# Kernel optimization log

Measured on AMD Instinct MI355X. Metric: run time of the kernel, lower is better.

The kernel has to match this reference:

```python
import jax, jax.numpy as jnp
import numpy as np

N, E, F, DH, R = 50000, 800000, 128, 128, 6  # nodes, edges, in-feat, hidden, relations (heads=1)
EPS = 1e-5
NEG_SLOPE = 0.01


def setup_inputs() -> dict:
    key = jax.random.key(0)
    ks = jax.random.split(key, 20)
    sF = 1.0 / np.sqrt(F)
    sD = 1.0 / np.sqrt(DH)
    return {
        "x": jax.random.normal(ks[0], (N, F), dtype=jnp.float32),
        "edge_index": jax.random.randint(ks[1], (2, E), 0, N, dtype=jnp.int64),
        "edge_type": jax.random.randint(ks[2], (E,), 0, R, dtype=jnp.int64),
        # RGCNConv params
        "rgcn_w": jax.random.normal(ks[3], (R, F, DH), dtype=jnp.float32) * sF,
        "rgcn_root": jax.random.normal(ks[4], (F, DH), dtype=jnp.float32) * sF,
        "rgcn_bias": jnp.zeros((DH,), dtype=jnp.float32),
        # TransformerConv params (heads=1, concat=True)
        "wq": jax.random.normal(ks[5], (DH, DH), dtype=jnp.float32) * sD,
        "bq": jnp.zeros((DH,), dtype=jnp.float32),
        "wk": jax.random.normal(ks[6], (DH, DH), dtype=jnp.float32) * sD,
        "bk": jnp.zeros((DH,), dtype=jnp.float32),
        "wv": jax.random.normal(ks[7], (DH, DH), dtype=jnp.float32) * sD,
        "bv": jnp.zeros((DH,), dtype=jnp.float32),
        "wskip": jax.random.normal(ks[8], (DH, DH), dtype=jnp.float32) * sD,
        "bskip": jnp.zeros((DH,), dtype=jnp.float32),
        # BatchNorm1d params (training-mode batch stats)
        "bn_gamma": jnp.ones((DH,), dtype=jnp.float32),
        "bn_beta": jnp.zeros((DH,), dtype=jnp.float32),
    }


def _rgcn(x, src, dst, edge_type, w, root, bias):
    # PyG RGCNConv: per-relation mean aggregation of x_j @ W_r over incoming edges, + root + bias
    out = x @ root + bias  # [N, DH]
    for r in range(R):
        m = (edge_type == r)
        xw = x @ w[r]  # [N, DH]
        msg = jnp.where(m[:, None], xw[src], 0.0)  # [E, DH]
        s = jax.ops.segment_sum(msg, dst, num_segments=N)
        cnt = jax.ops.segment_sum(m.astype(x.dtype), dst, num_segments=N)
        out = out + s / jnp.maximum(cnt, 1.0)[:, None]
    return out


def _transformer_conv(x, src, dst, wq, bq, wk, bk, wv, bv, wskip, bskip):
    # PyG TransformerConv, heads=1: edge-softmax attention over incoming edges + skip projection
    q = x @ wq + bq  # [N, DH]
    k = x @ wk + bk
    v = x @ wv + bv
    score = jnp.sum(q[dst] * k[src], axis=-1) / jnp.sqrt(jnp.asarray(DH, x.dtype))  # [E]
    smax = jax.ops.segment_max(score, dst, num_segments=N)  # -inf for empty segments (unused)
    a = jnp.exp(score - smax[dst])
    denom = jax.ops.segment_sum(a, dst, num_segments=N)
    alpha = a / denom[dst]  # every edge's dst has >=1 edge, denom > 0
    agg = jax.ops.segment_sum(alpha[:, None] * v[src], dst, num_segments=N)  # [N, DH]
    return agg + (x @ wskip + bskip)


def reference(x, edge_index, edge_type, rgcn_w, rgcn_root, rgcn_bias,
              wq, bq, wk, bk, wv, bv, wskip, bskip, bn_gamma, bn_beta):
    src, dst = edge_index[0], edge_index[1]
    h = _rgcn(x, src, dst, edge_type, rgcn_w, rgcn_root, rgcn_bias)
    h = _transformer_conv(h, src, dst, wq, bq, wk, bk, wv, bv, wskip, bskip)
    # BatchNorm1d (training: batch statistics, biased variance)
    mu = jnp.mean(h, axis=0)
    var = jnp.mean(jnp.square(h - mu), axis=0)
    h = bn_gamma * (h - mu) * jax.lax.rsqrt(var + EPS) + bn_beta
    return jnp.where(h > 0, h, NEG_SLOPE * h)
```

## Files before the change

### kernel.cpp

```cpp
#include <hip/hip_runtime.h>
#include <hip/hip_bf16.h>
#include <math.h>

#define FDIM 128
#define NREL 6

typedef _Float16 half8 __attribute__((ext_vector_type(8)));
typedef _Float16 h16x2 __attribute__((ext_vector_type(2)));
typedef float f32x4 __attribute__((ext_vector_type(4)));

#if __has_builtin(__builtin_amdgcn_fdot2)
#define FDOT2(A, B, C) __builtin_amdgcn_fdot2((A), (B), (C), false)
#else
#define FDOT2(A, B, C) ((float)(A)[0] * (float)(B)[0] + ((float)(A)[1] * (float)(B)[1] + (C)))
#endif

static __device__ __forceinline__ unsigned short f2h(float f) {
  union { _Float16 h; unsigned short u; } p; p.h = (_Float16)f; return p.u;
}

__global__ void cvt_x_kernel(const float* __restrict__ x, unsigned short* __restrict__ xh,
                             int n4) {
  int i = blockIdx.x * 256 + threadIdx.x;
  if (i < n4) {
    float4 v = ((const float4*)x)[i];
    union { _Float16 h[4]; uint2 u; } p;
    p.h[0] = (_Float16)v.x; p.h[1] = (_Float16)v.y;
    p.h[2] = (_Float16)v.z; p.h[3] = (_Float16)v.w;
    ((uint2*)xh)[i] = p.u;
  }
}

__global__ void cvt_wr_kernel(const float* __restrict__ root, const float* __restrict__ w,
                              unsigned short* __restrict__ bt) {
  int i = blockIdx.x * 256 + threadIdx.x;
  if (i < 896 * 128) {
    int n = i / 896, kk = i - n * 896;
    float v = (kk < 128) ? root[kk * 128 + n] : w[(long long)(kk - 128) * 128 + n];
    bt[i] = f2h(v);
  }
}

struct WPtrs { const float* W[4]; };
__global__ void cvt_wq_kernel(WPtrs wp, unsigned short* __restrict__ bt) {
  int i = blockIdx.x * 256 + threadIdx.x;
  if (i < 4 * 128 * 128) {
    int z = i >> 14;
    int r = i & 16383;
    int n = r >> 7, kk = r & 127;
    bt[i] = f2h(wp.W[z][kk * 128 + n]);
  }
}

struct GArgs {
  const unsigned short* Ax;
  const unsigned short* Aagg;
  const unsigned short* Bt;
  const float* bias[4];
  unsigned short* qh; unsigned short* kh; unsigned short* vh; float* sk;
  unsigned short* h;
  int M, K;
};

template <int MODE>
__launch_bounds__(256)
__global__ void gemm_mfma(GArgs g) {
  __shared__ unsigned short Ah[64 * 64];
  __shared__ unsigned short Bh[128 * 64];
  const int tid = threadIdx.x;
  const int lane = tid & 63;
  const int wid = tid >> 6;
  const int wm = wid >> 1, wn = wid & 1;
  const int lr = lane & 15, lk = lane >> 4;
  const int m0 = blockIdx.x * 64;
  const int z = (MODE == 1) ? blockIdx.z : 0;
  const unsigned short* Bt = g.Bt + (long long)z * 128 * g.K;
  const int K = g.K;
  const int M = g.M;

  f32x4 acc[2][4];
#pragma unroll
  for (int a = 0; a < 2; ++a)
#pragma unroll
    for (int b = 0; b < 4; ++b) { acc[a][b][0] = 0.f; acc[a][b][1] = 0.f; acc[a][b][2] = 0.f; acc[a][b][3] = 0.f; }

  for (int k0 = 0; k0 < K; k0 += 64) {
    __syncthreads();
#pragma unroll
    for (int p = 0; p < 2; ++p) {
      int idx = tid + 256 * p;
      int r = idx >> 3, c = idx & 7;
      int row = m0 + r; if (row > M - 1) row = M - 1;
      const unsigned short* srcp;
      if (MODE == 0)
        srcp = (k0 < 128) ? (g.Ax + (long long)row * 128 + k0 + c * 8)
                          : (g.Aagg + (long long)row * 768 + (k0 - 128) + c * 8);
      else
        srcp = g.Ax + (long long)row * 128 + k0 + c * 8;
      uint4 u = *(const uint4*)srcp;
      ((uint4*)Ah)[r * 8 + (c ^ (r & 7))] = u;
    }
#pragma unroll
    for (int p = 0; p < 4; ++p) {
      int idx = tid + 256 * p;
      int rn = idx >> 3, c = idx & 7;
      uint4 u = *(const uint4*)(Bt + (long long)rn * K + k0 + c * 8);
      ((uint4*)Bh)[rn * 8 + (c ^ (rn & 7))] = u;
    }
    __syncthreads();
#pragma unroll
    for (int ks = 0; ks < 2; ++ks) {
      half8 a[2], b[4];
#pragma unroll
      for (int fm = 0; fm < 2; ++fm) {
        int row = wm * 32 + fm * 16 + lr;
        a[fm] = *(const half8*)&((uint4*)Ah)[row * 8 + ((ks * 4 + lk) ^ (row & 7))];
      }
#pragma unroll
      for (int fn = 0; fn < 4; ++fn) {
        int col = wn * 64 + fn * 16 + lr;
        b[fn] = *(const half8*)&((uint4*)Bh)[col * 8 + ((ks * 4 + lk) ^ (col & 7))];
      }
#pragma unroll
      for (int fm = 0; fm < 2; ++fm)
#pragma unroll
        for (int fn = 0; fn < 4; ++fn)
          acc[fm][fn] = __builtin_amdgcn_mfma_f32_16x16x32_f16(a[fm], b[fn], acc[fm][fn], 0, 0, 0);
    }
  }

  const float CF = 0.08838834764831845f * 1.4426950408889634f;
  const float* bias = (MODE == 0) ? g.bias[0] : g.bias[z];
#pragma unroll
  for (int fm = 0; fm < 2; ++fm) {
#pragma unroll
    for (int fn = 0; fn < 4; ++fn) {
      int col = wn * 64 + fn * 16 + lr;
      float bv = bias[col];
#pragma unroll
      for (int j = 0; j < 4; ++j) {
        int row = m0 + wm * 32 + fm * 16 + lk * 4 + j;
        if (row < M) {
          float vv = acc[fm][fn][j] + bv;
          long long off = (long long)row * 128 + col;
          if (MODE == 0) {
            g.h[off] = f2h(vv);
          } else {
            if (z == 0) g.qh[off] = f2h(vv * CF);
            else if (z == 1) g.kh[off] = f2h(vv);
            else if (z == 2) g.vh[off] = f2h(vv);
            else g.sk[off] = vv;
          }
        }
      }
    }
  }
}

__global__ void hist_kernel(const int* __restrict__ dst, int* __restrict__ deg, int E) {
  int e = blockIdx.x * blockDim.x + threadIdx.x;
  if (e < E) atomicAdd(&deg[dst[e]], 1);
}

__launch_bounds__(1024)
__global__ void scan1(const int* __restrict__ deg, int* __restrict__ incl,
                      int* __restrict__ part, int n) {
  __shared__ int sh[1024];
  int tid = threadIdx.x;
  int i = blockIdx.x * 1024 + tid;
  sh[tid] = (i < n) ? deg[i] : 0;
  __syncthreads();
  for (int o = 1; o < 1024; o <<= 1) {
    int t = (tid >= o) ? sh[tid - o] : 0;
    __syncthreads();
    sh[tid] += t;
    __syncthreads();
  }
  if (i < n) incl[i] = sh[tid];
  if (tid == 1023) part[blockIdx.x] = sh[1023];
}

__global__ void scan2(int* part, int nb) {
  int lane = threadIdx.x;
  int run = 0;
  for (int b0 = 0; b0 < nb; b0 += 64) {
    int i = b0 + lane;
    int orig = (i < nb) ? part[i] : 0;
    int v = orig;
#pragma unroll
    for (int o = 1; o < 64; o <<= 1) {
      int t = __shfl_up(v, o);
      if (lane >= o) v += t;
    }
    if (i < nb) part[i] = run + v - orig;
    run += __shfl(v, 63);
  }
}

__global__ void scan3(const int* __restrict__ incl, const int* __restrict__ part,
                      int* __restrict__ offs, int n) {
  int i = blockIdx.x * blockDim.x + threadIdx.x;
  if (i < n) {
    offs[i + 1] = incl[i] + part[i >> 10];
    if (i == 0) offs[0] = 0;
  }
}

__global__ void scatter_kernel(const int* __restrict__ src, const int* __restrict__ dst,
                               const int* __restrict__ etype, const int* __restrict__ offs,
                               int* __restrict__ cur, int* __restrict__ csrc,
                               int* __restrict__ ctyp, int E) {
  int e = blockIdx.x * blockDim.x + threadIdx.x;
  if (e < E) {
    int d = dst[e];
    int p = offs[d] + atomicAdd(&cur[d], 1);
    csrc[p] = src[e];
    ctyp[p] = etype[e];
  }
}

__launch_bounds__(256)
__global__ void rgcn_agg(const unsigned short* __restrict__ xh, const int* __restrict__ offs,
                         const int* __restrict__ csrc, const int* __restrict__ ctyp,
                         unsigned short* __restrict__ aggh, int N) {
  int node = blockIdx.x * 4 + (threadIdx.x >> 6);
  if (node >= N) return;
  int lane = threadIdx.x & 63;
  int start = offs[node], end = offs[node + 1];

  float a0x = 0.f, a0y = 0.f, a1x = 0.f, a1y = 0.f, a2x = 0.f, a2y = 0.f;
  float a3x = 0.f, a3y = 0.f, a4x = 0.f, a4y = 0.f, a5x = 0.f, a5y = 0.f;
  int c0 = 0, c1 = 0, c2 = 0, c3 = 0, c4 = 0, c5 = 0;

#define ACC(T, XU)                                                         \
  {                                                                        \
    union { unsigned u; _Float16 h[2]; } cc; cc.u = (XU);                  \
    float fx = (float)cc.h[0], fy = (float)cc.h[1];                        \
    switch (T) {                                                           \
      case 0: a0x += fx; a0y += fy; ++c0; break;                           \
      case 1: a1x += fx; a1y += fy; ++c1; break;                           \
      case 2: a2x += fx; a2y += fy; ++c2; break;                           \
      case 3: a3x += fx; a3y += fy; ++c3; break;                           \
      case 4: a4x += fx; a4y += fy; ++c4; break;                           \
      default: a5x += fx; a5y += fy; ++c5; break;                          \
    }                                                                      \
  }

  int e = start;
  for (; e + 4 <= end; e += 4) {
    int s0 = csrc[e], s1 = csrc[e + 1], s2 = csrc[e + 2], s3 = csrc[e + 3];
    int t0 = __builtin_amdgcn_readfirstlane(ctyp[e]);
    int t1 = __builtin_amdgcn_readfirstlane(ctyp[e + 1]);
    int t2 = __builtin_amdgcn_readfirstlane(ctyp[e + 2]);
    int t3 = __builtin_amdgcn_readfirstlane(ctyp[e + 3]);
    unsigned x0 = ((const unsigned*)(xh + (long long)s0 * FDIM))[lane];
    unsigned x1 = ((const unsigned*)(xh + (long long)s1 * FDIM))[lane];
    unsigned x2 = ((const unsigned*)(xh + (long long)s2 * FDIM))[lane];
    unsigned x3 = ((const unsigned*)(xh + (long long)s3 * FDIM))[lane];
    ACC(t0, x0) ACC(t1, x1) ACC(t2, x2) ACC(t3, x3)
  }
  for (; e < end; ++e) {
    int s0 = csrc[e];
    int t0 = __builtin_amdgcn_readfirstlane(ctyp[e]);
    unsigned x0 = ((const unsigned*)(xh + (long long)s0 * FDIM))[lane];
    ACC(t0, x0)
  }
#undef ACC

  float i0 = c0 ? 1.f / (float)c0 : 0.f;
  float i1 = c1 ? 1.f / (float)c1 : 0.f;
  float i2 = c2 ? 1.f / (float)c2 : 0.f;
  float i3 = c3 ? 1.f / (float)c3 : 0.f;
  float i4 = c4 ? 1.f / (float)c4 : 0.f;
  float i5 = c5 ? 1.f / (float)c5 : 0.f;
  unsigned* ap = (unsigned*)(aggh + (long long)node * (NREL * FDIM));
  union { _Float16 h[2]; unsigned u; } p;
#define WR(ri, AX, AY, IV) { p.h[0] = (_Float16)((AX) * (IV)); p.h[1] = (_Float16)((AY) * (IV)); ap[(ri) * 64 + lane] = p.u; }
  WR(0, a0x, a0y, i0) WR(1, a1x, a1y, i1) WR(2, a2x, a2y, i2)
  WR(3, a3x, a3y, i3) WR(4, a4x, a4y, i4) WR(5, a5x, a5y, i5)
#undef WR
}

__launch_bounds__(256)
__global__ void attn_kernel(const unsigned short* __restrict__ qh,
                            const unsigned short* __restrict__ kh,
                            const unsigned short* __restrict__ vh,
                            const int* __restrict__ offs, const int* __restrict__ csrc,
                            float* __restrict__ out, int N) {
  int node = blockIdx.x * 4 + (threadIdx.x >> 6);
  if (node >= N) return;
  int lane = threadIdx.x & 63;
  int start = offs[node], end = offs[node + 1];
  int deg = end - start;
  if (deg <= 0) return;

  const int g16 = lane >> 4;
  const int f = lane & 15;

  union U4 { uint4 u; h16x2 h[4]; };
  U4 qf; qf.u = *(const uint4*)(qh + (long long)node * FDIM + f * 8);

  float m = -INFINITY, den = 0.f, acc0 = 0.f, acc1 = 0.f;

#define LOADQ(E0, S0, S1, S2, S3, KU, V0, V1, V2, V3)                        \
  {                                                                          \
    S0 = csrc[(E0) + (g16 ^ 0)];                                             \
    S1 = csrc[(E0) + (g16 ^ 1)];                                             \
    S2 = csrc[(E0) + (g16 ^ 2)];                                             \
    S3 = csrc[(E0) + (g16 ^ 3)];                                             \
    KU = *(const uint4*)(kh + (long long)S0 * FDIM + f * 8);                 \
    V0 = ((const unsigned*)(vh + (long long)S0 * FDIM))[lane];               \
    V1 = ((const unsigned*)(vh + (long long)S1 * FDIM))[lane];               \
    V2 = ((const unsigned*)(vh + (long long)S2 * FDIM))[lane];               \
    V3 = ((const unsigned*)(vh + (long long)S3 * FDIM))[lane];               \
  }

#define PROCESS(KU, V0, V1, V2, V3, MASKED, M0, M1, M2, M3)                  \
  {                                                                          \
    U4 kf; kf.u = KU;                                                        \
    float pd = FDOT2(qf.h[0], kf.h[0], 0.f);                                 \
    pd = FDOT2(qf.h[1], kf.h[1], pd);                                        \
    pd = FDOT2(qf.h[2], kf.h[2], pd);                                        \
    pd = FDOT2(qf.h[3], kf.h[3], pd);                                        \
    pd += __shfl_xor(pd, 1);  pd += __shfl_xor(pd, 2);                       \
    pd += __shfl_xor(pd, 4);  pd += __shfl_xor(pd, 8);                       \
    float sc0 = pd;                                        \
    float sc1 = __shfl_xor(pd, 16);                        \
    float sc2 = __shfl_xor(pd, 32);                        \
    float sc3 = __shfl_xor(pd, 48);                        \
    if (MASKED) {                                                            \
      if (!(M0)) sc0 = -INFINITY;                                            \
      if (!(M1)) sc1 = -INFINITY;                                            \
      if (!(M2)) sc2 = -INFINITY;                                            \
      if (!(M3)) sc3 = -INFINITY;                                            \
    }                                                                        \
    float mx = fmaxf(fmaxf(sc0, sc1), fmaxf(sc2, sc3));                      \
    float mn = fmaxf(m, mx);                                                 \
    float scl = exp2f(m - mn);                                               \
    float a0 = exp2f(sc0 - mn), a1 = exp2f(sc1 - mn);                        \
    float a2 = exp2f(sc2 - mn), a3 = exp2f(sc3 - mn);                        \
    den = den * scl + ((a0 + a1) + (a2 + a3));                               \
    union { unsigned u; _Float16 h[2]; } w0, w1, w2, w3;                     \
    w0.u = V0; w1.u = V1; w2.u = V2; w3.u = V3;                              \
    acc0 = acc0 * scl + a0 * (float)w0.h[0] + a1 * (float)w1.h[0]            \
                      + a2 * (float)w2.h[0] + a3 * (float)w3.h[0];           \
    acc1 = acc1 * scl + a0 * (float)w0.h[1] + a1 * (float)w1.h[1]            \
                      + a2 * (float)w2.h[1] + a3 * (float)w3.h[1];           \
    m = mn;                                                                  \
  }

  int nfull4 = deg & ~3;
  int e = start;
  if (nfull4 > 0) {
    int sA0, sA1, sA2, sA3; uint4 kA; unsigned vA0, vA1, vA2, vA3;
    LOADQ(e, sA0, sA1, sA2, sA3, kA, vA0, vA1, vA2, vA3)
    for (; e < start + nfull4; e += 4) {
      int sB0, sB1, sB2, sB3; uint4 kB; unsigned vB0, vB1, vB2, vB3;
      bool more = (e + 4 < start + nfull4);
      if (more) LOADQ(e + 4, sB0, sB1, sB2, sB3, kB, vB0, vB1, vB2, vB3)
      PROCESS(kA, vA0, vA1, vA2, vA3, false, 1, 1, 1, 1)
      if (more) { kA = kB; vA0 = vB0; vA1 = vB1; vA2 = vB2; vA3 = vB3; }
    }
  }
  int rem = deg & 3;
  if (rem) {
    int e0 = start + nfull4;
    int j0 = g16 ^ 0, j1 = g16 ^ 1, j2 = g16 ^ 2, j3 = g16 ^ 3;
    int sT0 = csrc[e0 + (j0 < rem ? j0 : 0)];
    int sT1 = csrc[e0 + (j1 < rem ? j1 : 0)];
    int sT2 = csrc[e0 + (j2 < rem ? j2 : 0)];
    int sT3 = csrc[e0 + (j3 < rem ? j3 : 0)];
    uint4 kT = *(const uint4*)(kh + (long long)sT0 * FDIM + f * 8);
    unsigned vT0 = ((const unsigned*)(vh + (long long)sT0 * FDIM))[lane];
    unsigned vT1 = ((const unsigned*)(vh + (long long)sT1 * FDIM))[lane];
    unsigned vT2 = ((const unsigned*)(vh + (long long)sT2 * FDIM))[lane];
    unsigned vT3 = ((const unsigned*)(vh + (long long)sT3 * FDIM))[lane];
    PROCESS(kT, vT0, vT1, vT2, vT3, true, j0 < rem, j1 < rem, j2 < rem, j3 < rem)
  }
#undef LOADQ
#undef PROCESS

  float inv = 1.f / den;
  float2* op = (float2*)(out + (long long)node * FDIM);
  float2 o = op[lane];
  o.x += acc0 * inv;
  o.y += acc1 * inv;
  op[lane] = o;
}

__launch_bounds__(128)
__global__ void bn_stats(const float* __restrict__ x, float* __restrict__ gsum,
                         float* __restrict__ gsq, int N) {
  int d = threadIdx.x;
  float s = 0.f, qq = 0.f;
  for (int r = blockIdx.x; r < N; r += gridDim.x) {
    float vv = x[(long long)r * FDIM + d];
    s += vv;
    qq += vv * vv;
  }
  atomicAdd(&gsum[d], s);
  atomicAdd(&gsq[d], qq);
}

__global__ void bn_final(const float* __restrict__ gsum, const float* __restrict__ gsq,
                         const float* __restrict__ gamma, const float* __restrict__ beta,
                         float* __restrict__ ss, int N) {
  int d = threadIdx.x;
  if (d < FDIM) {
    float mean = gsum[d] / (float)N;
    float var = gsq[d] / (float)N - mean * mean;
    var = fmaxf(var, 0.f);
    float sc = gamma[d] * rsqrtf(var + 1e-5f);
    ss[d] = sc;
    ss[FDIM + d] = beta[d] - mean * sc;
  }
}

__global__ void bn_apply(float* __restrict__ x, const float* __restrict__ ss, long long total4) {
  long long i = (long long)blockIdx.x * blockDim.x + threadIdx.x;
  if (i < total4) {
    int d0 = (int)((i * 4) & (FDIM - 1));
    float4 vv = ((const float4*)x)[i];
    float y0 = ss[d0 + 0] * vv.x + ss[FDIM + d0 + 0];
    float y1 = ss[d0 + 1] * vv.y + ss[FDIM + d0 + 1];
    float y2 = ss[d0 + 2] * vv.z + ss[FDIM + d0 + 2];
    float y3 = ss[d0 + 3] * vv.w + ss[FDIM + d0 + 3];
    vv.x = (y0 > 0.f) ? y0 : 0.01f * y0;
    vv.y = (y1 > 0.f) ? y1 : 0.01f * y1;
    vv.z = (y2 > 0.f) ? y2 : 0.01f * y2;
    vv.w = (y3 > 0.f) ? y3 : 0.01f * y3;
    ((float4*)x)[i] = vv;
  }
}

extern "C" void kernel_launch(void* const* d_in, const int* in_sizes, int n_in,
                              void* d_out, int out_size, void* d_ws, size_t ws_size,
                              hipStream_t stream) {
  const float* x         = (const float*)d_in[0];
  const int*   ei        = (const int*)d_in[1];
  const int*   etype     = (const int*)d_in[2];
  const float* rgcn_w    = (const float*)d_in[3];
  const float* rgcn_root = (const float*)d_in[4];
  const float* rgcn_bias = (const float*)d_in[5];
  const float* wq = (const float*)d_in[6];  const float* bq = (const float*)d_in[7];
  const float* wk = (const float*)d_in[8];  const float* bk = (const float*)d_in[9];
  const float* wv = (const float*)d_in[10]; const float* bv = (const float*)d_in[11];
  const float* wsk = (const float*)d_in[12]; const float* bsk = (const float*)d_in[13];
  const float* gamma = (const float*)d_in[14]; const float* beta = (const float*)d_in[15];

  const int N = in_sizes[0] / FDIM;
  const int E = in_sizes[1] / 2;
  const int* src = ei;
  const int* dst = ei + E;

  char* base = (char*)d_ws;
  size_t off = 0;
  auto alloc = [&](size_t bytes) -> char* {
    char* p = base + off;
    off += (bytes + 255) & ~(size_t)255;
    return p;
  };
  unsigned short* aggh = (unsigned short*)alloc((size_t)N * (NREL * FDIM) * 2);
  unsigned short* qbuf = aggh;
  unsigned short* kbuf = aggh + (size_t)N * FDIM;
  unsigned short* vbuf = aggh + 2 * (size_t)N * FDIM;
  unsigned short* xh   = (unsigned short*)alloc((size_t)N * FDIM * 2);
  unsigned short* hh   = (unsigned short*)alloc((size_t)N * FDIM * 2);
  unsigned short* btR  = (unsigned short*)alloc((size_t)896 * 128 * 2);
  unsigned short* btQ  = (unsigned short*)alloc((size_t)4 * 128 * 128 * 2);
  int* deg  = (int*)alloc((size_t)2 * N * 4);
  int* cur  = deg + N;
  int* offs = (int*)alloc((size_t)(N + 1) * 4);
  int* incl = (int*)alloc((size_t)N * 4);
  int* part = (int*)alloc((size_t)64 * 4);
  int* csrc = (int*)alloc((size_t)E * 4);
  int* ctyp = (int*)alloc((size_t)E * 4);
  float* gsum = (float*)alloc((size_t)(128 + 128 + 256) * 4);
  float* gsq  = gsum + FDIM;
  float* ss   = gsum + 2 * FDIM;

  float* out = (float*)d_out;

  hipMemsetAsync(deg, 0, (size_t)2 * N * sizeof(int), stream);
  hipMemsetAsync(gsum, 0, (size_t)2 * FDIM * sizeof(float), stream);

  int n4 = N * FDIM / 4;
  cvt_x_kernel<<<(n4 + 255) / 256, 256, 0, stream>>>(x, xh, n4);
  cvt_wr_kernel<<<(896 * 128 + 255) / 256, 256, 0, stream>>>(rgcn_root, rgcn_w, btR);
  WPtrs wp; wp.W[0] = wq; wp.W[1] = wk; wp.W[2] = wv; wp.W[3] = wsk;
  cvt_wq_kernel<<<(4 * 128 * 128 + 255) / 256, 256, 0, stream>>>(wp, btQ);

  hist_kernel<<<(E + 255) / 256, 256, 0, stream>>>(dst, deg, E);
  int nb = (N + 1023) / 1024;
  scan1<<<nb, 1024, 0, stream>>>(deg, incl, part, N);
  scan2<<<1, 64, 0, stream>>>(part, nb);
  scan3<<<(N + 255) / 256, 256, 0, stream>>>(incl, part, offs, N);
  scatter_kernel<<<(E + 255) / 256, 256, 0, stream>>>(src, dst, etype, offs, cur, csrc, ctyp, E);

  const int nodeBlocks = (N + 3) / 4;
  const int gemmBlocks = (N + 63) / 64;

  rgcn_agg<<<nodeBlocks, 256, 0, stream>>>(xh, offs, csrc, ctyp, aggh, N);

  GArgs g0 = {};
  g0.Ax = xh; g0.Aagg = aggh; g0.Bt = btR;
  g0.bias[0] = rgcn_bias;
  g0.h = hh; g0.M = N; g0.K = 896;
  gemm_mfma<0><<<dim3(gemmBlocks, 1, 1), 256, 0, stream>>>(g0);

  GArgs g1 = {};
  g1.Ax = hh; g1.Bt = btQ;
  g1.bias[0] = bq; g1.bias[1] = bk; g1.bias[2] = bv; g1.bias[3] = bsk;
  g1.qh = qbuf; g1.kh = kbuf; g1.vh = vbuf; g1.sk = out;
  g1.M = N; g1.K = 128;
  gemm_mfma<1><<<dim3(gemmBlocks, 1, 4), 256, 0, stream>>>(g1);

  attn_kernel<<<nodeBlocks, 256, 0, stream>>>(qbuf, kbuf, vbuf, offs, csrc, out, N);

  bn_stats<<<512, 128, 0, stream>>>(out, gsum, gsq, N);
  bn_final<<<1, 128, 0, stream>>>(gsum, gsq, gamma, beta, ss, N);
  long long total4 = (long long)N * FDIM / 4;
  bn_apply<<<(int)((total4 + 255) / 256), 256, 0, stream>>>(out, ss, total4);
}
```

Measured before the change: 356.4 us.

## Sort CSR by (dst, relation) and aggregate per-relation segments without type array

The edge CSR is now keyed by destination node times relation, so the histogram, scan and scatter run over N*6 buckets and the per-edge type array is dropped. The RGCN aggregation walks each relation's contiguous segment with a two-deep software prefetch of gathered rows. This removes the per-edge type load and the switch over six accumulator pairs. In exchange the count and scan arrays grow sixfold, the scan grows to about 300 blocks, and scan2 must handle up to 512 partials with a single 64-thread block.

After: 374.3 us. 5.0% more time.

```diff
diff --git a/kernel.cpp b/kernel.cpp
--- a/kernel.cpp
+++ b/kernel.cpp
@@ -157,9 +157,10 @@
   }
 }
 
-__global__ void hist_kernel(const int* __restrict__ dst, int* __restrict__ deg, int E) {
+__global__ void hist_kernel(const int* __restrict__ dst, const int* __restrict__ etype,
+                            int* __restrict__ cnt, int E) {
   int e = blockIdx.x * blockDim.x + threadIdx.x;
-  if (e < E) atomicAdd(&deg[dst[e]], 1);
+  if (e < E) atomicAdd(&cnt[dst[e] * NREL + etype[e]], 1);
 }
 
 __launch_bounds__(1024)
@@ -207,90 +208,63 @@
 }
 
 __global__ void scatter_kernel(const int* __restrict__ src, const int* __restrict__ dst,
-                               const int* __restrict__ etype, const int* __restrict__ offs,
-                               int* __restrict__ cur, int* __restrict__ csrc,
-                               int* __restrict__ ctyp, int E) {
+                               const int* __restrict__ etype, const int* __restrict__ offs6,
+                               int* __restrict__ cur, int* __restrict__ csrc, int E) {
   int e = blockIdx.x * blockDim.x + threadIdx.x;
   if (e < E) {
-    int d = dst[e];
-    int p = offs[d] + atomicAdd(&cur[d], 1);
+    int key = dst[e] * NREL + etype[e];
+    int p = offs6[key] + atomicAdd(&cur[key], 1);
     csrc[p] = src[e];
-    ctyp[p] = etype[e];
   }
 }
 
 __launch_bounds__(256)
-__global__ void rgcn_agg(const unsigned short* __restrict__ xh, const int* __restrict__ offs,
-                         const int* __restrict__ csrc, const int* __restrict__ ctyp,
+__global__ void rgcn_agg(const unsigned short* __restrict__ xh, const int* __restrict__ offs6,
+                         const int* __restrict__ csrc,
                          unsigned short* __restrict__ aggh, int N) {
   int node = blockIdx.x * 4 + (threadIdx.x >> 6);
   if (node >= N) return;
   int lane = threadIdx.x & 63;
-  int start = offs[node], end = offs[node + 1];
-
-  float a0x = 0.f, a0y = 0.f, a1x = 0.f, a1y = 0.f, a2x = 0.f, a2y = 0.f;
-  float a3x = 0.f, a3y = 0.f, a4x = 0.f, a4y = 0.f, a5x = 0.f, a5y = 0.f;
-  int c0 = 0, c1 = 0, c2 = 0, c3 = 0, c4 = 0, c5 = 0;
-
-#define ACC(T, XU)                                                         \
-  {                                                                        \
-    union { unsigned u; _Float16 h[2]; } cc; cc.u = (XU);                  \
-    float fx = (float)cc.h[0], fy = (float)cc.h[1];                        \
-    switch (T) {                                                           \
-      case 0: a0x += fx; a0y += fy; ++c0; break;                           \
-      case 1: a1x += fx; a1y += fy; ++c1; break;                           \
-      case 2: a2x += fx; a2y += fy; ++c2; break;                           \
-      case 3: a3x += fx; a3y += fy; ++c3; break;                           \
-      case 4: a4x += fx; a4y += fy; ++c4; break;                           \
-      default: a5x += fx; a5y += fy; ++c5; break;                          \
-    }                                                                      \
-  }
-
-  int e = start;
-  for (; e + 4 <= end; e += 4) {
-    int s0 = csrc[e], s1 = csrc[e + 1], s2 = csrc[e + 2], s3 = csrc[e + 3];
-    int t0 = __builtin_amdgcn_readfirstlane(ctyp[e]);
-    int t1 = __builtin_amdgcn_readfirstlane(ctyp[e + 1]);
-    int t2 = __builtin_amdgcn_readfirstlane(ctyp[e + 2]);
-    int t3 = __builtin_amdgcn_readfirstlane(ctyp[e + 3]);
-    unsigned x0 = ((const unsigned*)(xh + (long long)s0 * FDIM))[lane];
-    unsigned x1 = ((const unsigned*)(xh + (long long)s1 * FDIM))[lane];
-    unsigned x2 = ((const unsigned*)(xh + (long long)s2 * FDIM))[lane];
-    unsigned x3 = ((const unsigned*)(xh + (long long)s3 * FDIM))[lane];
-    ACC(t0, x0) ACC(t1, x1) ACC(t2, x2) ACC(t3, x3)
-  }
-  for (; e < end; ++e) {
-    int s0 = csrc[e];
-    int t0 = __builtin_amdgcn_readfirstlane(ctyp[e]);
-    unsigned x0 = ((const unsigned*)(xh + (long long)s0 * FDIM))[lane];
-    ACC(t0, x0)
-  }
-#undef ACC
-
-  float i0 = c0 ? 1.f / (float)c0 : 0.f;
-  float i1 = c1 ? 1.f / (float)c1 : 0.f;
-  float i2 = c2 ? 1.f / (float)c2 : 0.f;
-  float i3 = c3 ? 1.f / (float)c3 : 0.f;
-  float i4 = c4 ? 1.f / (float)c4 : 0.f;
-  float i5 = c5 ? 1.f / (float)c5 : 0.f;
+  const int* bptr = offs6 + node * NREL;
+  const int b0 = bptr[0];
+  const int b6 = bptr[NREL];
   unsigned* ap = (unsigned*)(aggh + (long long)node * (NREL * FDIM));
-  union { _Float16 h[2]; unsigned u; } p;
-#define WR(ri, AX, AY, IV) { p.h[0] = (_Float16)((AX) * (IV)); p.h[1] = (_Float16)((AY) * (IV)); ap[(ri) * 64 + lane] = p.u; }
-  WR(0, a0x, a0y, i0) WR(1, a1x, a1y, i1) WR(2, a2x, a2y, i2)
-  WR(3, a3x, a3y, i3) WR(4, a4x, a4y, i4) WR(5, a5x, a5y, i5)
-#undef WR
+
+  int e = b0;
+  unsigned pf0 = 0, pf1 = 0;
+  if (e < b6)     pf0 = ((const unsigned*)(xh + (long long)csrc[e] * FDIM))[lane];
+  if (e + 1 < b6) pf1 = ((const unsigned*)(xh + (long long)csrc[e + 1] * FDIM))[lane];
+
+  int bprev = b0;
+#pragma unroll
+  for (int r = 0; r < NREL; ++r) {
+    int bnext = bptr[r + 1];
+    float ax = 0.f, ay = 0.f;
+    for (; e < bnext; ++e) {
+      union { unsigned u; _Float16 h[2]; } c; c.u = pf0;
+      pf0 = pf1;
+      if (e + 2 < b6) pf1 = ((const unsigned*)(xh + (long long)csrc[e + 2] * FDIM))[lane];
+      ax += (float)c.h[0]; ay += (float)c.h[1];
+    }
+    int cnt = bnext - bprev;
+    float inv = cnt ? 1.f / (float)cnt : 0.f;
+    union { _Float16 h[2]; unsigned u; } p;
+    p.h[0] = (_Float16)(ax * inv); p.h[1] = (_Float16)(ay * inv);
+    ap[r * 64 + lane] = p.u;
+    bprev = bnext;
+  }
 }
 
 __launch_bounds__(256)
 __global__ void attn_kernel(const unsigned short* __restrict__ qh,
                             const unsigned short* __restrict__ kh,
                             const unsigned short* __restrict__ vh,
-                            const int* __restrict__ offs, const int* __restrict__ csrc,
+                            const int* __restrict__ offs6, const int* __restrict__ csrc,
                             float* __restrict__ out, int N) {
   int node = blockIdx.x * 4 + (threadIdx.x >> 6);
   if (node >= N) return;
   int lane = threadIdx.x & 63;
-  int start = offs[node], end = offs[node + 1];
+  int start = offs6[node * NREL], end = offs6[node * NREL + NREL];
   int deg = end - start;
   if (deg <= 0) return;
 
@@ -452,6 +426,7 @@
   const int E = in_sizes[1] / 2;
   const int* src = ei;
   const int* dst = ei + E;
+  const int NK = N * NREL;
 
   char* base = (char*)d_ws;
   size_t off = 0;
@@ -468,20 +443,19 @@
   unsigned short* hh   = (unsigned short*)alloc((size_t)N * FDIM * 2);
   unsigned short* btR  = (unsigned short*)alloc((size_t)896 * 128 * 2);
   unsigned short* btQ  = (unsigned short*)alloc((size_t)4 * 128 * 128 * 2);
-  int* deg  = (int*)alloc((size_t)2 * N * 4);
-  int* cur  = deg + N;
-  int* offs = (int*)alloc((size_t)(N + 1) * 4);
-  int* incl = (int*)alloc((size_t)N * 4);
-  int* part = (int*)alloc((size_t)64 * 4);
+  int* cnt6 = (int*)alloc((size_t)2 * NK * 4);
+  int* cur  = cnt6 + NK;
+  int* offs6 = (int*)alloc((size_t)(NK + 1) * 4);
+  int* incl = (int*)alloc((size_t)NK * 4);
+  int* part = (int*)alloc((size_t)512 * 4);
   int* csrc = (int*)alloc((size_t)E * 4);
-  int* ctyp = (int*)alloc((size_t)E * 4);
   float* gsum = (float*)alloc((size_t)(128 + 128 + 256) * 4);
   float* gsq  = gsum + FDIM;
   float* ss   = gsum + 2 * FDIM;
 
   float* out = (float*)d_out;
 
-  hipMemsetAsync(deg, 0, (size_t)2 * N * sizeof(int), stream);
+  hipMemsetAsync(cnt6, 0, (size_t)2 * NK * sizeof(int), stream);
   hipMemsetAsync(gsum, 0, (size_t)2 * FDIM * sizeof(float), stream);
 
   int n4 = N * FDIM / 4;
@@ -490,17 +464,17 @@
   WPtrs wp; wp.W[0] = wq; wp.W[1] = wk; wp.W[2] = wv; wp.W[3] = wsk;
   cvt_wq_kernel<<<(4 * 128 * 128 + 255) / 256, 256, 0, stream>>>(wp, btQ);
 
-  hist_kernel<<<(E + 255) / 256, 256, 0, stream>>>(dst, deg, E);
-  int nb = (N + 1023) / 1024;
-  scan1<<<nb, 1024, 0, stream>>>(deg, incl, part, N);
+  hist_kernel<<<(E + 255) / 256, 256, 0, stream>>>(dst, etype, cnt6, E);
+  int nb = (NK + 1023) / 1024;
+  scan1<<<nb, 1024, 0, stream>>>(cnt6, incl, part, NK);
   scan2<<<1, 64, 0, stream>>>(part, nb);
-  scan3<<<(N + 255) / 256, 256, 0, stream>>>(incl, part, offs, N);
-  scatter_kernel<<<(E + 255) / 256, 256, 0, stream>>>(src, dst, etype, offs, cur, csrc, ctyp, E);
+  scan3<<<(NK + 255) / 256, 256, 0, stream>>>(incl, part, offs6, NK);
+  scatter_kernel<<<(E + 255) / 256, 256, 0, stream>>>(src, dst, etype, offs6, cur, csrc, E);
 
   const int nodeBlocks = (N + 3) / 4;
   const int gemmBlocks = (N + 63) / 64;
 
-  rgcn_agg<<<nodeBlocks, 256, 0, stream>>>(xh, offs, csrc, ctyp, aggh, N);
+  rgcn_agg<<<nodeBlocks, 256, 0, stream>>>(xh, offs6, csrc, aggh, N);
 
   GArgs g0 = {};
   g0.Ax = xh; g0.Aagg = aggh; g0.Bt = btR;
@@ -515,7 +489,7 @@
   g1.M = N; g1.K = 128;
   gemm_mfma<1><<<dim3(gemmBlocks, 1, 4), 256, 0, stream>>>(g1);
 
-  attn_kernel<<<nodeBlocks, 256, 0, stream>>>(qbuf, kbuf, vbuf, offs, csrc, out, N);
+  attn_kernel<<<nodeBlocks, 256, 0, stream>>>(qbuf, kbuf, vbuf, offs6, csrc, out, N);
 
   bn_stats<<<512, 128, 0, stream>>>(out, gsum, gsq, N);
   bn_final<<<1, 128, 0, stream>>>(gsum, gsq, gamma, beta, ss, N);
```
